# Performance work log

Measured on AMD Instinct MI355X. Metric: run time of the kernel, lower is better.

## Reference

```python
import jax, jax.numpy as jnp
import numpy as np

N_NODES = 100000
N_EDGES = 1600000
HIDDEN = 64
IN_CH = 6  # 3 (direction) + 3 (node feature part)
BN_EPS = 1e-5


def setup_inputs() -> dict:
    key = jax.random.key(0)
    ks = jax.random.split(key, 16)
    inp = {
        "x": jax.random.normal(ks[0], (N_NODES, 3), dtype=jnp.float32),
        "pos": jax.random.normal(ks[1], (N_NODES, 3), dtype=jnp.float32),
        "edge_index": jax.random.randint(ks[2], (2, N_EDGES), 0, N_NODES, dtype=jnp.int64),
    }
    dims = [IN_CH, HIDDEN, HIDDEN, HIDDEN]
    for i in range(3):
        din, dout = dims[i], dims[i + 1]
        inp[f"W{i+1}"] = jax.random.normal(ks[3 + 4 * i], (din, dout), dtype=jnp.float32) * (1.0 / np.sqrt(din))
        inp[f"b{i+1}"] = jnp.zeros((dout,), dtype=jnp.float32)
        inp[f"g{i+1}"] = jnp.ones((dout,), dtype=jnp.float32)   # BN gamma
        inp[f"be{i+1}"] = jnp.zeros((dout,), dtype=jnp.float32)  # BN beta
    return inp


def _mlp_layer(h, W, b, g, be):
    # Linear -> ReLU -> BatchNorm1d (training mode, biased variance like torch)
    h = jax.nn.relu(h @ W + b)
    mu = jnp.mean(h, axis=0)
    var = jnp.mean((h - mu) ** 2, axis=0)
    return g * (h - mu) * jax.lax.rsqrt(var + BN_EPS) + be


def reference(x, pos, edge_index, W1, b1, g1, be1, W2, b2, g2, be2, W3, b3, g3, be3):
    n = x.shape[0]
    xp = jnp.concatenate([pos, x], axis=1)             # [N, 3+F]
    src, dst = edge_index[0], edge_index[1]            # j = src, i = dst (PyG source_to_target)
    x_j = xp[src]                                      # [E, 3+F]
    x_i = xp[dst]
    direction = x_j[:, :3] - x_i[:, :3]                # [E, 3]
    # NOTE: source uses torch.norm with no dim => single global scalar norm
    direction = direction / jnp.linalg.norm(direction)
    h = jnp.concatenate([direction, x_i[:, 3:]], axis=-1)  # [E, IN_CH]
    h = _mlp_layer(h, W1, b1, g1, be1)
    h = _mlp_layer(h, W2, b2, g2, be2)
    h = _mlp_layer(h, W3, b3, g3, be3)                 # [E, HIDDEN]
    out = jax.ops.segment_max(h, dst, num_segments=n)  # scatter-max aggregation
    out = jnp.where(jnp.isfinite(out), out, 0.0)       # PyG fills empty segments with 0
    return out
```

## Files before the change

kernel.cpp:

```cpp
#include <hip/hip_runtime.h>
#include <stdint.h>

typedef unsigned short u16;
typedef unsigned int u32;
typedef __attribute__((ext_vector_type(8))) short short8;
typedef __attribute__((ext_vector_type(4))) float floatx4;

#define BN_EPS 1e-5f
#define NPB 256
#define NBMAX 512

__device__ __forceinline__ float bf2f(u16 u) { return __uint_as_float(((unsigned)u) << 16); }
__device__ __forceinline__ u16 f2bf(float f) {
  unsigned u = __float_as_uint(f);
  u += 0x7FFFu + ((u >> 16) & 1u);
  return (u16)(u >> 16);
}
__device__ __forceinline__ u32 fkey(float f) {
  unsigned u = __float_as_uint(f);
  return (u >> 31) ? ~u : (u | 0x80000000u);
}
__device__ __forceinline__ float funkey(u32 k) {
  return (k & 0x80000000u) ? __uint_as_float(k ^ 0x80000000u) : __uint_as_float(~k);
}

__global__ void k_init(float* __restrict__ stats, u32* __restrict__ bucketTotal) {
  for (int i = threadIdx.x; i < 1024; i += blockDim.x) stats[i] = 0.f;
  for (int i = threadIdx.x; i < NBMAX + 1; i += blockDim.x) bucketTotal[i] = 0u;
}

__global__ void k_norm_hist(const int* __restrict__ ei, const float* __restrict__ pos,
                            int E, int NB, float* __restrict__ stats,
                            u32* __restrict__ bucketTotal) {
  __shared__ u32 lh[NBMAX];
  __shared__ float red[16];
  for (int i = threadIdx.x; i < NB; i += blockDim.x) lh[i] = 0u;
  __syncthreads();
  int tid = blockIdx.x * blockDim.x + threadIdx.x;
  int stride = gridDim.x * blockDim.x;
  float acc = 0.f;
  for (int e = tid; e < E; e += stride) {
    int s = ei[e], d = ei[E + e];
    float d0 = pos[3 * s + 0] - pos[3 * d + 0];
    float d1 = pos[3 * s + 1] - pos[3 * d + 1];
    float d2 = pos[3 * s + 2] - pos[3 * d + 2];
    acc = fmaf(d0, d0, acc);
    acc = fmaf(d1, d1, acc);
    acc = fmaf(d2, d2, acc);
    atomicAdd(&lh[d >> 8], 1u);
  }
#pragma unroll
  for (int off = 32; off > 0; off >>= 1) acc += __shfl_down(acc, off, 64);
  if ((threadIdx.x & 63) == 0) red[threadIdx.x >> 6] = acc;
  __syncthreads();
  if (threadIdx.x == 0) {
    float s = 0.f;
    for (int w = 0; w < (int)(blockDim.x >> 6); w++) s += red[w];
    atomicAdd(&stats[0], s);
  }
  for (int i = threadIdx.x; i < NB; i += blockDim.x)
    if (lh[i]) atomicAdd(&bucketTotal[i], lh[i]);
}

__global__ void k_scan(const u32* __restrict__ bucketTotal, u32* __restrict__ base,
                       u32* __restrict__ cursor, int NB) {
  if (threadIdx.x == 0 && blockIdx.x == 0) {
    u32 run = 0;
    for (int b = 0; b < NB; b++) {
      base[b] = run;
      cursor[b] = run;
      run += bucketTotal[b];
    }
    base[NB] = run;
  }
}

__global__ void k_place(const int* __restrict__ ei, int E, int NB,
                        u32* __restrict__ cursor, u32* __restrict__ sorted) {
  __shared__ u32 lh[NBMAX];
  __shared__ u32 lbase[NBMAX];
  for (int i = threadIdx.x; i < NB; i += blockDim.x) lh[i] = 0u;
  __syncthreads();
  int tid = blockIdx.x * blockDim.x + threadIdx.x;
  int stride = gridDim.x * blockDim.x;
  for (int e = tid; e < E; e += stride) atomicAdd(&lh[ei[E + e] >> 8], 1u);
  __syncthreads();
  for (int i = threadIdx.x; i < NB; i += blockDim.x) {
    u32 c = lh[i];
    lbase[i] = c ? atomicAdd(&cursor[i], c) : 0u;
    lh[i] = 0u;
  }
  __syncthreads();
  for (int e = tid; e < E; e += stride) {
    int d = ei[E + e];
    int b = d >> 8;
    u32 slot = lbase[b] + atomicAdd(&lh[b], 1u);
    sorted[slot] = ((u32)e << 8) | (u32)(d & 255);
  }
}

__global__ __launch_bounds__(512) void k_bucket_max(
    const u32* __restrict__ sorted, const u32* __restrict__ base,
    const u16* __restrict__ h, const float* __restrict__ sc3,
    const float* __restrict__ sh3, float* __restrict__ outf, int N) {
  __shared__ u32 tile[NPB * 64];
  for (int i = threadIdx.x; i < NPB * 64; i += blockDim.x) tile[i] = 0u;
  int b = blockIdx.x;
  u32 start = base[b];
  int cnt = (int)(base[b + 1] - start);
  int t = threadIdx.x;
  int es = t >> 3;
  int c0 = (t & 7) * 8;
  float sc[8], sh[8];
#pragma unroll
  for (int j = 0; j < 8; j++) { sc[j] = sc3[c0 + j]; sh[j] = sh3[c0 + j]; }
  __syncthreads();

  for (int i0 = 0; i0 < cnt; i0 += 256) {
    u32 pk[4];
    uint4 raw[4];
    int ok[4];
#pragma unroll
    for (int u_ = 0; u_ < 4; u_++) {
      int sl = i0 + u_ * 64 + es;
      ok[u_] = sl < cnt;
      pk[u_] = ok[u_] ? sorted[start + sl] : 0u;
    }
#pragma unroll
    for (int u_ = 0; u_ < 4; u_++)
      if (ok[u_]) raw[u_] = *(const uint4*)(h + (long)(pk[u_] >> 8) * 64 + c0);
#pragma unroll
    for (int u_ = 0; u_ < 4; u_++) {
      if (!ok[u_]) continue;
      int ln = (int)(pk[u_] & 255u);
      unsigned w[4] = {raw[u_].x, raw[u_].y, raw[u_].z, raw[u_].w};
      u32 key[8];
#pragma unroll
      for (int p = 0; p < 4; p++) {
        float v0 = bf2f((u16)(w[p] & 0xFFFFu));
        float v1 = bf2f((u16)(w[p] >> 16));
        key[2 * p] = fkey(fmaf(v0, sc[2 * p], sh[2 * p]));
        key[2 * p + 1] = fkey(fmaf(v1, sc[2 * p + 1], sh[2 * p + 1]));
      }
#pragma unroll
      for (int jj = 0; jj < 8; jj++) {
        int j = (jj + es) & 7;
        atomicMax(&tile[ln * 64 + c0 + j], key[j]);
      }
    }
  }
  __syncthreads();
  int node0 = b * NPB;
  for (int l = t; l < NPB * 64; l += blockDim.x) {
    int node = node0 + (l >> 6);
    if (node < N) {
      u32 k = tile[l];
      outf[(long)node * 64 + (l & 63)] = (k == 0u) ? 0.f : funkey(k);
    }
  }
}

__global__ __launch_bounds__(256) void k_layer1(
    const int* __restrict__ ei, const float* __restrict__ pos,
    const float* __restrict__ x, const float* __restrict__ W1,
    const float* __restrict__ b1, u16* __restrict__ h,
    const float* __restrict__ stats, float* __restrict__ gsum,
    float* __restrict__ gsq, int E) {
  __shared__ float in6[6][256];
  __shared__ float ssum[64], ssq[64];
  float invn = 1.0f / sqrtf(stats[0]);
  int t = threadIdx.x;
  int lane = t & 63;
  int wv = t >> 6;
  float w[6];
#pragma unroll
  for (int k = 0; k < 6; k++) w[k] = W1[k * 64 + lane];
  float bias = b1[lane];
  float psum = 0.f, psq = 0.f;

  int chunks = (E + 255) >> 8;
  for (int c = blockIdx.x; c < chunks; c += gridDim.x) {
    long e0 = (long)c << 8;
    int e = (int)e0 + t;
    float v[6] = {0.f, 0.f, 0.f, 0.f, 0.f, 0.f};
    if (e < E) {
      int s = ei[e], d = ei[E + e];
      float p0 = pos[3 * s + 0], p1 = pos[3 * s + 1], p2 = pos[3 * s + 2];
      float q0 = pos[3 * d + 0], q1 = pos[3 * d + 1], q2 = pos[3 * d + 2];
      v[0] = (p0 - q0) * invn;
      v[1] = (p1 - q1) * invn;
      v[2] = (p2 - q2) * invn;
      v[3] = x[3 * d + 0];
      v[4] = x[3 * d + 1];
      v[5] = x[3 * d + 2];
    }
    __syncthreads();
#pragma unroll
    for (int k = 0; k < 6; k++) in6[k][t] = v[k];
    __syncthreads();
    int lim = E - (int)e0;
    if (lim > 256) lim = 256;
    int base = wv * 64;
#pragma unroll 4
    for (int i = 0; i < 64; i++) {
      int el = base + i;
      if (el >= lim) break;
      float acc = bias;
#pragma unroll
      for (int k = 0; k < 6; k++) acc = fmaf(in6[k][el], w[k], acc);
      acc = fmaxf(acc, 0.f);
      u16 hb = f2bf(acc);
      h[(e0 + el) * 64 + lane] = hb;
      float hf = bf2f(hb);
      psum += hf;
      psq = fmaf(hf, hf, psq);
    }
  }
  if (t < 64) { ssum[t] = 0.f; ssq[t] = 0.f; }
  __syncthreads();
  atomicAdd(&ssum[lane], psum);
  atomicAdd(&ssq[lane], psq);
  __syncthreads();
  if (t < 64) {
    atomicAdd(&gsum[t], ssum[t]);
    atomicAdd(&gsq[t], ssq[t]);
  }
}

__global__ void k_fin(const float* __restrict__ gsum, const float* __restrict__ gsq,
                      const float* __restrict__ g, const float* __restrict__ be,
                      float* __restrict__ scale, float* __restrict__ shift, float invE) {
  int c = threadIdx.x;
  float mu = gsum[c] * invE;
  float var = gsq[c] * invE - mu * mu;
  float s = g[c] * rsqrtf(var + BN_EPS);
  scale[c] = s;
  shift[c] = be[c] - mu * s;
}

__global__ __launch_bounds__(256) void k_layer_mfma(
    u16* h, const float* __restrict__ W, const float* __restrict__ b,
    const float* __restrict__ scale_in, const float* __restrict__ shift_in,
    float* __restrict__ gsum, float* __restrict__ gsq, int E) {
  int lane = threadIdx.x & 63;
  int m = lane & 15;
  int q = lane >> 4;

  short8 bf[4][2];
  float bias[4];
#pragma unroll
  for (int t = 0; t < 4; t++) {
    int n = t * 16 + m;
    float bb = b[n];
    for (int k = 0; k < 64; k++) bb = fmaf(shift_in[k], W[k * 64 + n], bb);
    bias[t] = bb;
#pragma unroll
    for (int s = 0; s < 2; s++)
#pragma unroll
      for (int j = 0; j < 8; j++) {
        int k = s * 32 + q * 8 + j;
        bf[t][s][j] = (short)f2bf(W[k * 64 + n] * scale_in[k]);
      }
  }

  float psum[4] = {0.f, 0.f, 0.f, 0.f}, psq[4] = {0.f, 0.f, 0.f, 0.f};

  int tiles = E >> 4;
  int gw = ((int)blockIdx.x * (blockDim.x >> 6)) + (threadIdx.x >> 6);
  int nw = (int)gridDim.x * (blockDim.x >> 6);

  for (int tile = gw; tile < tiles; tile += nw) {
    long e0 = (long)tile * 16;
    const u16* rowp = h + (e0 + m) * 64 + q * 8;
    short8 a0 = *(const short8*)(rowp);
    short8 a1 = *(const short8*)(rowp + 32);
    floatx4 acc[4];
#pragma unroll
    for (int t = 0; t < 4; t++) acc[t] = (floatx4){0.f, 0.f, 0.f, 0.f};
#pragma unroll
    for (int t = 0; t < 4; t++)
      acc[t] = __builtin_amdgcn_mfma_f32_16x16x32_bf16(a0, bf[t][0], acc[t], 0, 0, 0);
#pragma unroll
    for (int t = 0; t < 4; t++)
      acc[t] = __builtin_amdgcn_mfma_f32_16x16x32_bf16(a1, bf[t][1], acc[t], 0, 0, 0);

#pragma unroll
    for (int t = 0; t < 4; t++) {
#pragma unroll
      for (int r = 0; r < 4; r++) {
        float v = acc[t][r] + bias[t];
        v = fmaxf(v, 0.f);
        u16 hb = f2bf(v);
        h[(e0 + q * 4 + r) * 64 + t * 16 + m] = hb;
        float hf = bf2f(hb);
        psum[t] += hf;
        psq[t] = fmaf(hf, hf, psq[t]);
      }
    }
  }

#pragma unroll
  for (int t = 0; t < 4; t++) {
    psum[t] += __shfl_xor(psum[t], 16, 64);
    psum[t] += __shfl_xor(psum[t], 32, 64);
    psq[t] += __shfl_xor(psq[t], 16, 64);
    psq[t] += __shfl_xor(psq[t], 32, 64);
  }
  __shared__ float ssum[64], ssq[64];
  if (threadIdx.x < 64) { ssum[threadIdx.x] = 0.f; ssq[threadIdx.x] = 0.f; }
  __syncthreads();
  if (q == 0) {
#pragma unroll
    for (int t = 0; t < 4; t++) {
      atomicAdd(&ssum[t * 16 + m], psum[t]);
      atomicAdd(&ssq[t * 16 + m], psq[t]);
    }
  }
  __syncthreads();
  if (threadIdx.x < 64) {
    atomicAdd(&gsum[threadIdx.x], ssum[threadIdx.x]);
    atomicAdd(&gsq[threadIdx.x], ssq[threadIdx.x]);
  }
}

__global__ void k_initout(float* __restrict__ outf, long n, float* __restrict__ stats,
                          u32* __restrict__ bucketTotal) {
  long i = (long)blockIdx.x * blockDim.x + threadIdx.x;
  long stride = (long)gridDim.x * blockDim.x;
  for (long j = i; j < n; j += stride) outf[j] = __uint_as_float(0xFF800000u);
  if (i < 1024) stats[i] = 0.f;
  if (i < NBMAX + 1) bucketTotal[i] = 0u;
}
__global__ void k_scatter(const int* __restrict__ ei, const u16* __restrict__ h,
                          const float* __restrict__ scale, const float* __restrict__ shift,
                          float* outf, int E) {
  int lane = threadIdx.x & 63;
  int gw = ((int)blockIdx.x * (blockDim.x >> 6)) + (threadIdx.x >> 6);
  int nw = (int)gridDim.x * (blockDim.x >> 6);
  float sc = scale[lane], sh = shift[lane];
  for (int e = gw; e < E; e += nw) {
    int d = ei[E + e];
    float v = fmaf(bf2f(h[(long)e * 64 + lane]), sc, sh);
    float* addr = outf + (long)d * 64 + lane;
    if (v >= 0.f)
      atomicMax((int*)addr, __float_as_int(v));
    else
      atomicMin((unsigned int*)addr, __float_as_uint(v));
  }
}
__global__ void k_out(float* __restrict__ outf, long n) {
  long i = (long)blockIdx.x * blockDim.x + threadIdx.x;
  long stride = (long)gridDim.x * blockDim.x;
  for (long j = i; j < n; j += stride) {
    float v = outf[j];
    unsigned u = __float_as_uint(v);
    if ((u & 0x7F800000u) == 0x7F800000u) v = 0.f;
    outf[j] = v;
  }
}

extern "C" void kernel_launch(void* const* d_in, const int* in_sizes, int n_in,
                              void* d_out, int out_size, void* d_ws, size_t ws_size,
                              hipStream_t stream) {
  const float* x = (const float*)d_in[0];
  const float* pos = (const float*)d_in[1];
  const int* ei = (const int*)d_in[2];
  const float* W1 = (const float*)d_in[3];
  const float* b1 = (const float*)d_in[4];
  const float* g1 = (const float*)d_in[5];
  const float* be1 = (const float*)d_in[6];
  const float* W2 = (const float*)d_in[7];
  const float* b2 = (const float*)d_in[8];
  const float* g2 = (const float*)d_in[9];
  const float* be2 = (const float*)d_in[10];
  const float* W3 = (const float*)d_in[11];
  const float* b3 = (const float*)d_in[12];
  const float* g3 = (const float*)d_in[13];
  const float* be3 = (const float*)d_in[14];

  int N = in_sizes[0] / 3;
  int E = in_sizes[2] / 2;
  int NB = (N + NPB - 1) / NPB;
  long n_out = (long)N * 64;

  char* wsb = (char*)d_ws;
  u16* h = (u16*)wsb;
  size_t off = (size_t)E * 64 * 2;
  float* stats = (float*)(wsb + off);
  off += 1024 * 4;
  u32* bucketTotal = (u32*)(wsb + off);
  off += (NBMAX + 1) * 4;
  u32* baseArr = (u32*)(wsb + off);
  off += (NBMAX + 1) * 4;
  u32* cursor = (u32*)(wsb + off);
  off += NBMAX * 4;
  u32* sorted = (u32*)(wsb + off);
  off += (size_t)E * 4;
  size_t need = off;

  float* gsum1 = stats + 64, * gsq1 = stats + 128;
  float* gsum2 = stats + 192, * gsq2 = stats + 256;
  float* gsum3 = stats + 320, * gsq3 = stats + 384;
  float* sc1 = stats + 512, * sh1 = stats + 576;
  float* sc2 = stats + 640, * sh2 = stats + 704;
  float* sc3 = stats + 768, * sh3 = stats + 832;

  float* outf = (float*)d_out;
  float invE = 1.0f / (float)E;
  bool binned = (ws_size >= need) && (NB <= NBMAX);

  if (binned) {
    k_init<<<1, 1024, 0, stream>>>(stats, bucketTotal);
    k_norm_hist<<<256, 256, 0, stream>>>(ei, pos, E, NB, stats, bucketTotal);
    k_scan<<<1, 64, 0, stream>>>(bucketTotal, baseArr, cursor, NB);
    k_place<<<256, 256, 0, stream>>>(ei, E, NB, cursor, sorted);
    k_layer1<<<1024, 256, 0, stream>>>(ei, pos, x, W1, b1, h, stats, gsum1, gsq1, E);
    k_fin<<<1, 64, 0, stream>>>(gsum1, gsq1, g1, be1, sc1, sh1, invE);
    k_layer_mfma<<<1024, 256, 0, stream>>>(h, W2, b2, sc1, sh1, gsum2, gsq2, E);
    k_fin<<<1, 64, 0, stream>>>(gsum2, gsq2, g2, be2, sc2, sh2, invE);
    k_layer_mfma<<<1024, 256, 0, stream>>>(h, W3, b3, sc2, sh2, gsum3, gsq3, E);
    k_fin<<<1, 64, 0, stream>>>(gsum3, gsq3, g3, be3, sc3, sh3, invE);
    k_bucket_max<<<NB, 512, 0, stream>>>(sorted, baseArr, h, sc3, sh3, outf, N);
  } else {
    k_initout<<<4096, 256, 0, stream>>>(outf, n_out, stats, bucketTotal);
    k_norm_hist<<<256, 256, 0, stream>>>(ei, pos, E, NB <= NBMAX ? NB : 1, stats, bucketTotal);
    k_layer1<<<1024, 256, 0, stream>>>(ei, pos, x, W1, b1, h, stats, gsum1, gsq1, E);
    k_fin<<<1, 64, 0, stream>>>(gsum1, gsq1, g1, be1, sc1, sh1, invE);
    k_layer_mfma<<<1024, 256, 0, stream>>>(h, W2, b2, sc1, sh1, gsum2, gsq2, E);
    k_fin<<<1, 64, 0, stream>>>(gsum2, gsq2, g2, be2, sc2, sh2, invE);
    k_layer_mfma<<<1024, 256, 0, stream>>>(h, W3, b3, sc2, sh2, gsum3, gsq3, E);
    k_fin<<<1, 64, 0, stream>>>(gsum3, gsq3, g3, be3, sc3, sh3, invE);
    k_scatter<<<2048, 256, 0, stream>>>(ei, h, sc3, sh3, outf, E);
    k_out<<<2048, 256, 0, stream>>>(outf, n_out);
  }
}
```

Measured before the change: 512.8 us.

## Replace LDS atomic bucket max with per-node CSR sort and wave max

A per-bucket counting sort now turns the bucketed edge list into node-contiguous CSR order with per-node offsets. The max aggregation then gives each node to one wave, which loops over that node's edges and keeps a register fmax per channel. This removes the shared-memory atomicMax traffic and the orderable-key encoding. In exchange it adds an extra kernel, an extra pass over the edge ids, and a serial per-edge gather whose latency is only partly hidden.

```diff
diff --git a/kernel.cpp b/kernel.cpp
--- a/kernel.cpp
+++ b/kernel.cpp
@@ -15,13 +15,6 @@
   unsigned u = __float_as_uint(f);
   u += 0x7FFFu + ((u >> 16) & 1u);
   return (u16)(u >> 16);
-}
-__device__ __forceinline__ u32 fkey(float f) {
-  unsigned u = __float_as_uint(f);
-  return (u >> 31) ? ~u : (u | 0x80000000u);
-}
-__device__ __forceinline__ float funkey(u32 k) {
-  return (k & 0x80000000u) ? __uint_as_float(k ^ 0x80000000u) : __uint_as_float(~k);
 }
 
 __global__ void k_init(float* __restrict__ stats, u32* __restrict__ bucketTotal) {
@@ -99,64 +92,66 @@
   }
 }
 
-__global__ __launch_bounds__(512) void k_bucket_max(
-    const u32* __restrict__ sorted, const u32* __restrict__ base,
+__global__ __launch_bounds__(256) void k_bucket_sort(
+    const u32* __restrict__ sp, const u32* __restrict__ bbase,
+    u32* __restrict__ sorted2, u32* __restrict__ nodeBase) {
+  __shared__ u32 hist[NPB];
+  __shared__ u32 sbase[NPB];
+  int b = blockIdx.x;
+  u32 start = bbase[b];
+  int cnt = (int)(bbase[b + 1] - start);
+  int t = threadIdx.x;
+  hist[t] = 0u;
+  __syncthreads();
+  for (int i = t; i < cnt; i += 256) atomicAdd(&hist[sp[start + i] & 255u], 1u);
+  __syncthreads();
+  u32 hv = hist[t];
+  sbase[t] = hv;
+  __syncthreads();
+  for (int off = 1; off < 256; off <<= 1) {
+    u32 xx = (t >= off) ? sbase[t - off] : 0u;
+    __syncthreads();
+    sbase[t] += xx;
+    __syncthreads();
+  }
+  u32 excl = sbase[t] - hv;
+  __syncthreads();
+  sbase[t] = start + excl;
+  nodeBase[b * NPB + t] = start + excl;
+  hist[t] = 0u;
+  __syncthreads();
+  for (int i = t; i < cnt; i += 256) {
+    u32 pk = sp[start + i];
+    u32 ln = pk & 255u;
+    u32 slot = sbase[ln] + atomicAdd(&hist[ln], 1u);
+    sorted2[slot] = pk >> 8;
+  }
+}
+
+__global__ __launch_bounds__(256) void k_node_max(
+    const u32* __restrict__ sorted2, const u32* __restrict__ nodeBase,
     const u16* __restrict__ h, const float* __restrict__ sc3,
     const float* __restrict__ sh3, float* __restrict__ outf, int N) {
-  __shared__ u32 tile[NPB * 64];
-  for (int i = threadIdx.x; i < NPB * 64; i += blockDim.x) tile[i] = 0u;
-  int b = blockIdx.x;
-  u32 start = base[b];
-  int cnt = (int)(base[b + 1] - start);
-  int t = threadIdx.x;
-  int es = t >> 3;
-  int c0 = (t & 7) * 8;
-  float sc[8], sh[8];
-#pragma unroll
-  for (int j = 0; j < 8; j++) { sc[j] = sc3[c0 + j]; sh[j] = sh3[c0 + j]; }
-  __syncthreads();
-
-  for (int i0 = 0; i0 < cnt; i0 += 256) {
-    u32 pk[4];
-    uint4 raw[4];
-    int ok[4];
-#pragma unroll
-    for (int u_ = 0; u_ < 4; u_++) {
-      int sl = i0 + u_ * 64 + es;
-      ok[u_] = sl < cnt;
-      pk[u_] = ok[u_] ? sorted[start + sl] : 0u;
-    }
-#pragma unroll
-    for (int u_ = 0; u_ < 4; u_++)
-      if (ok[u_]) raw[u_] = *(const uint4*)(h + (long)(pk[u_] >> 8) * 64 + c0);
-#pragma unroll
-    for (int u_ = 0; u_ < 4; u_++) {
-      if (!ok[u_]) continue;
-      int ln = (int)(pk[u_] & 255u);
-      unsigned w[4] = {raw[u_].x, raw[u_].y, raw[u_].z, raw[u_].w};
-      u32 key[8];
-#pragma unroll
-      for (int p = 0; p < 4; p++) {
-        float v0 = bf2f((u16)(w[p] & 0xFFFFu));
-        float v1 = bf2f((u16)(w[p] >> 16));
-        key[2 * p] = fkey(fmaf(v0, sc[2 * p], sh[2 * p]));
-        key[2 * p + 1] = fkey(fmaf(v1, sc[2 * p + 1], sh[2 * p + 1]));
+  int lane = threadIdx.x & 63;
+  int w = ((int)blockIdx.x * (blockDim.x >> 6)) + (threadIdx.x >> 6);
+  int nw = (int)gridDim.x * (blockDim.x >> 6);
+  float sc = sc3[lane], sh = sh3[lane];
+  for (int n = w; n < N; n += nw) {
+    u32 s0 = nodeBase[n];
+    int cnt = (int)(nodeBase[n + 1] - s0);
+    float v = -3.4e38f;
+    for (int i0 = 0; i0 < cnt; i0 += 64) {
+      int lim = cnt - i0;
+      if (lim > 64) lim = 64;
+      u32 myid = (lane < lim) ? sorted2[s0 + i0 + lane] : 0u;
+#pragma unroll 4
+      for (int i = 0; i < lim; i++) {
+        u32 e = __shfl(myid, i, 64);
+        float hf = bf2f(h[(long)e * 64 + lane]);
+        v = fmaxf(v, fmaf(hf, sc, sh));
       }
-#pragma unroll
-      for (int jj = 0; jj < 8; jj++) {
-        int j = (jj + es) & 7;
-        atomicMax(&tile[ln * 64 + c0 + j], key[j]);
-      }
-    }
-  }
-  __syncthreads();
-  int node0 = b * NPB;
-  for (int l = t; l < NPB * 64; l += blockDim.x) {
-    int node = node0 + (l >> 6);
-    if (node < N) {
-      u32 k = tile[l];
-      outf[(long)node * 64 + (l & 63)] = (k == 0u) ? 0.f : funkey(k);
-    }
+    }
+    outf[(long)n * 64 + lane] = (cnt == 0) ? 0.f : v;
   }
 }
 
@@ -394,8 +389,12 @@
   off += (NBMAX + 1) * 4;
   u32* cursor = (u32*)(wsb + off);
   off += NBMAX * 4;
-  u32* sorted = (u32*)(wsb + off);
+  u32* sortedPk = (u32*)(wsb + off);
   off += (size_t)E * 4;
+  u32* sorted2 = (u32*)(wsb + off);
+  off += (size_t)E * 4;
+  u32* nodeBase = (u32*)(wsb + off);
+  off += ((size_t)NBMAX * NPB + 1) * 4;
   size_t need = off;
 
   float* gsum1 = stats + 64, * gsq1 = stats + 128;
@@ -413,14 +412,15 @@
     k_init<<<1, 1024, 0, stream>>>(stats, bucketTotal);
     k_norm_hist<<<256, 256, 0, stream>>>(ei, pos, E, NB, stats, bucketTotal);
     k_scan<<<1, 64, 0, stream>>>(bucketTotal, baseArr, cursor, NB);
-    k_place<<<256, 256, 0, stream>>>(ei, E, NB, cursor, sorted);
+    k_place<<<256, 256, 0, stream>>>(ei, E, NB, cursor, sortedPk);
+    k_bucket_sort<<<NB, 256, 0, stream>>>(sortedPk, baseArr, sorted2, nodeBase);
     k_layer1<<<1024, 256, 0, stream>>>(ei, pos, x, W1, b1, h, stats, gsum1, gsq1, E);
     k_fin<<<1, 64, 0, stream>>>(gsum1, gsq1, g1, be1, sc1, sh1, invE);
     k_layer_mfma<<<1024, 256, 0, stream>>>(h, W2, b2, sc1, sh1, gsum2, gsq2, E);
     k_fin<<<1, 64, 0, stream>>>(gsum2, gsq2, g2, be2, sc2, sh2, invE);
     k_layer_mfma<<<1024, 256, 0, stream>>>(h, W3, b3, sc2, sh2, gsum3, gsq3, E);
     k_fin<<<1, 64, 0, stream>>>(gsum3, gsq3, g3, be3, sc3, sh3, invE);
-    k_bucket_max<<<NB, 512, 0, stream>>>(sorted, baseArr, h, sc3, sh3, outf, N);
+    k_node_max<<<1024, 256, 0, stream>>>(sorted2, nodeBase, h, sc3, sh3, outf, N);
   } else {
     k_initout<<<4096, 256, 0, stream>>>(outf, n_out, stats, bucketTotal);
     k_norm_hist<<<256, 256, 0, stream>>>(ei, pos, E, NB <= NBMAX ? NB : 1, stats, bucketTotal);
```

Measured after the change: 591.3 us. +15.3%, slower.
